# Kernel optimization log

Hardware: AMD Instinct MI355X
Metric: run time of the kernel (lower is better)

## Reference

```python
import jax, jax.numpy as jnp
import numpy as np

ALPHA = 0.2  # LeakyReLU negative slope
B, L, FIN, FOUT = 128, 512, 128, 128

def setup_inputs() -> dict:
    key = jax.random.key(0)
    k1, k2, k3, k4, k5 = jax.random.split(key, 5)
    h = jax.random.normal(k1, (B, L, FIN), jnp.float32)
    W = jax.random.normal(k2, (FIN, FOUT), jnp.float32) * (1.0 / np.sqrt(FIN))
    a = jax.random.normal(k3, (2 * FOUT,), jnp.float32) * (1.0 / np.sqrt(2 * FOUT))
    edge_bias = jax.random.normal(k4, (B, L, L), jnp.float32) * 0.1
    adj_mask = jax.random.uniform(k5, (L, L)) > 0.3
    adj_mask = adj_mask | jnp.eye(L, dtype=bool)  # self-loops avoid fully-masked rows
    return {"h": h, "W": W, "a": a, "edge_bias": edge_bias, "adj_mask": adj_mask}

def reference(h, W, a, edge_bias, adj_mask):
    # Wh: [B, L, Fout]
    Wh = jnp.einsum('blf,fo->blo', h, W)
    Fout = W.shape[1]
    # a([Wh_i, Wh_j]) == Wh_i @ a[:Fout] + Wh_j @ a[Fout:]  (avoids O(B*L*L*2F) concat)
    ei = Wh @ a[:Fout]   # [B, L]  (target i contribution)
    ej = Wh @ a[Fout:]   # [B, L]  (source j contribution)
    e = jax.nn.leaky_relu(ei[:, :, None] + ej[:, None, :], ALPHA) + edge_bias  # [B, L, L]
    e = jnp.where(adj_mask[None, :, :], e, -jnp.inf)
    att = jax.nn.softmax(e, axis=-1)  # dropout=0.0 -> identity
    h_prime = jnp.einsum('bij,bjo->bio', att, Wh)  # [B, L, Fout]
    return jax.nn.elu(h_prime)  # concat=True branch
```

## Files before the change

### kernel.cpp

```cpp
#include <hip/hip_runtime.h>
#include <string.h>

#define ALPHA 0.2f

typedef short short8 __attribute__((ext_vector_type(8)));
typedef float floatx4 __attribute__((ext_vector_type(4)));
typedef int intx4 __attribute__((ext_vector_type(4)));
typedef unsigned short ushort4v __attribute__((ext_vector_type(4)));

__device__ inline unsigned short f2bf(float f) {
    unsigned int v; __builtin_memcpy(&v, &f, 4);
    v = v + 0x7FFFu + ((v >> 16) & 1u);
    return (unsigned short)(v >> 16);
}

__device__ inline floatx4 ntload_f4(const float* p) {
    return __builtin_nontemporal_load((const floatx4*)p);
}

__global__ __launch_bounds__(256) void wh_kernel(const float* __restrict__ h,
                                                 const float* __restrict__ W,
                                                 const float* __restrict__ a,
                                                 unsigned short* __restrict__ wht,
                                                 float* __restrict__ ei,
                                                 float* __restrict__ ej)
{
    __shared__ __align__(16) unsigned short h_s[128][136];
    __shared__ __align__(16) unsigned short w_s[128][136];
    __shared__ float a_s[256];
    const int tid  = threadIdx.x;
    const int lane = tid & 63;
    const int wv   = tid >> 6;
    const int quad = lane >> 4;
    const int l16  = lane & 15;
    const int r0   = blockIdx.x * 128;
    const int b    = r0 >> 9;
    const int jb   = r0 & 511;

    const float* hbase = h + (size_t)r0 * 128;
    for (int it = 0; it < 16; ++it) {
        int idx4 = it * 256 + tid;
        floatx4 v = *(const floatx4*)(hbase + idx4 * 4);
        int row = idx4 >> 5;
        int col = (idx4 & 31) * 4;
        ushort4v u;
        for (int e = 0; e < 4; ++e) u[e] = f2bf(v[e]);
        *(ushort4v*)&h_s[row][col] = u;
    }
    for (int it = 0; it < 64; ++it) {
        int idx = it * 256 + tid;
        w_s[idx & 127][idx >> 7] = f2bf(W[idx]);
    }
    a_s[tid] = a[tid];
    __syncthreads();

    floatx4 acc[8][2];
    for (int mo = 0; mo < 8; ++mo)
        for (int n = 0; n < 2; ++n) acc[mo][n] = (floatx4)0.f;

    for (int kk = 0; kk < 4; ++kk) {
        short8 bfr[2];
        for (int n = 0; n < 2; ++n)
            bfr[n] = *(const short8*)&h_s[wv * 32 + n * 16 + l16][kk * 32 + quad * 8];
        for (int mo = 0; mo < 8; ++mo) {
            short8 afr = *(const short8*)&w_s[mo * 16 + l16][kk * 32 + quad * 8];
            acc[mo][0] = __builtin_amdgcn_mfma_f32_16x16x32_bf16(afr, bfr[0], acc[mo][0], 0, 0, 0);
            acc[mo][1] = __builtin_amdgcn_mfma_f32_16x16x32_bf16(afr, bfr[1], acc[mo][1], 0, 0, 0);
        }
    }

    for (int n = 0; n < 2; ++n) {
        float si = 0.f, sj = 0.f;
        for (int mo = 0; mo < 8; ++mo)
            for (int r = 0; r < 4; ++r) {
                int o = mo * 16 + quad * 4 + r;
                float v = acc[mo][n][r];
                si += v * a_s[o];
                sj += v * a_s[128 + o];
            }
        si += __shfl_xor(si, 16); si += __shfl_xor(si, 32);
        sj += __shfl_xor(sj, 16); sj += __shfl_xor(sj, 32);
        if (quad == 0) {
            int j = jb + wv * 32 + n * 16 + l16;
            ei[b * 512 + j] = si;
            ej[b * 512 + j] = sj;
        }
    }

    for (int mo = 0; mo < 8; ++mo)
        for (int n = 0; n < 2; ++n)
            for (int r = 0; r < 4; ++r) {
                int o = mo * 16 + quad * 4 + r;
                int j = jb + wv * 32 + n * 16 + l16;
                wht[(size_t)b * 65536 + o * 512 + j] = f2bf(acc[mo][n][r]);
            }
}

__global__ __launch_bounds__(512, 4) void attn_kernel(const unsigned short* __restrict__ wht,
                                                      const float* __restrict__ ei,
                                                      const float* __restrict__ ej,
                                                      const float* __restrict__ bias,
                                                      const int* __restrict__ adj,
                                                      float* __restrict__ out)
{
    __shared__ __align__(16) unsigned short p_s[64][520];
    __shared__ float ei_s[64];
    __shared__ float s_row[64];

    const int tid  = threadIdx.x;
    const int lane = tid & 63;
    const int wv   = tid >> 6;
    const int quad = lane >> 4;
    const int l16  = lane & 15;

    const int n  = blockIdx.x;
    const int x  = n & 7;
    const int r  = n >> 3;
    const int b  = x * 16 + (r >> 3);
    const int i0 = (r & 7) * 64;

    const float* bp = bias + ((size_t)(b * 512 + i0 + wv * 8)) * 512;
    const int*   ap = adj + (i0 + wv * 8) * 512;
    floatx4 bb0 = ntload_f4(bp + lane * 4);
    floatx4 bb1 = ntload_f4(bp + 256 + lane * 4);
    intx4   mm0 = *(const intx4*)(ap + lane * 4);
    intx4   mm1 = *(const intx4*)(ap + 256 + lane * 4);

    const floatx4 ejv0 = *(const floatx4*)(ej + b * 512 + lane * 4);
    const floatx4 ejv1 = *(const floatx4*)(ej + b * 512 + 256 + lane * 4);
    if (tid < 64) ei_s[tid] = ei[b * 512 + i0 + tid];
    __syncthreads();

    float rsum[8];

#pragma unroll
    for (int rr = 0; rr < 8; ++rr) {
        floatx4 nb0, nb1; intx4 nm0, nm1;
        if (rr < 7) {
            nb0 = ntload_f4(bp + 512 + lane * 4);
            nb1 = ntload_f4(bp + 768 + lane * 4);
            nm0 = *(const intx4*)(ap + 512 + lane * 4);
            nm1 = *(const intx4*)(ap + 768 + lane * 4);
        }
        const int il = wv * 8 + rr;
        const float eiv = ei_s[il];
        float sm = 0.f;
        ushort4v p0, p1;
#pragma unroll
        for (int e = 0; e < 4; ++e) {
            float xv = eiv + ejv0[e];
            xv = fmaxf(xv, ALPHA * xv);
            xv += bb0[e];
            float p = __expf(xv);
            p = (mm0[e] != 0) ? p : 0.f;
            sm += p;
            p0[e] = f2bf(p);
        }
#pragma unroll
        for (int e = 0; e < 4; ++e) {
            float xv = eiv + ejv1[e];
            xv = fmaxf(xv, ALPHA * xv);
            xv += bb1[e];
            float p = __expf(xv);
            p = (mm1[e] != 0) ? p : 0.f;
            sm += p;
            p1[e] = f2bf(p);
        }
        *(ushort4v*)&p_s[il][lane * 4]       = p0;
        *(ushort4v*)&p_s[il][256 + lane * 4] = p1;
        rsum[rr] = sm;
        bb0 = nb0; bb1 = nb1; mm0 = nm0; mm1 = nm1;
        bp += 512; ap += 512;
    }

#pragma unroll
    for (int rr = 0; rr < 8; ++rr)
        for (int off = 32; off; off >>= 1)
            rsum[rr] += __shfl_xor(rsum[rr], off);
    if (lane == 0)
#pragma unroll
        for (int rr = 0; rr < 8; ++rr) s_row[wv * 8 + rr] = rsum[rr];
    __syncthreads();

    floatx4 acc[4];
#pragma unroll
    for (int m = 0; m < 4; ++m) acc[m] = (floatx4)0.f;

    const unsigned short* wb = wht + (size_t)b * 65536 + (wv * 16 + l16) * 512 + quad * 8;
    short8 bf = *(const short8*)(wb);
#pragma unroll
    for (int k16 = 0; k16 < 16; ++k16) {
        int ko = k16 * 32 + quad * 8;
        short8 nbf;
        if (k16 < 15) nbf = *(const short8*)(wb + (k16 + 1) * 32);
        short8 af0 = *(const short8*)&p_s[l16][ko];
        short8 af1 = *(const short8*)&p_s[16 + l16][ko];
        short8 af2 = *(const short8*)&p_s[32 + l16][ko];
        short8 af3 = *(const short8*)&p_s[48 + l16][ko];
        acc[0] = __builtin_amdgcn_mfma_f32_16x16x32_bf16(af0, bf, acc[0], 0, 0, 0);
        acc[1] = __builtin_amdgcn_mfma_f32_16x16x32_bf16(af1, bf, acc[1], 0, 0, 0);
        acc[2] = __builtin_amdgcn_mfma_f32_16x16x32_bf16(af2, bf, acc[2], 0, 0, 0);
        acc[3] = __builtin_amdgcn_mfma_f32_16x16x32_bf16(af3, bf, acc[3], 0, 0, 0);
        bf = nbf;
    }

#pragma unroll
    for (int m = 0; m < 4; ++m)
#pragma unroll
        for (int rr2 = 0; rr2 < 4; ++rr2) {
            int il = m * 16 + quad * 4 + rr2;
            int o  = wv * 16 + l16;
            float v = acc[m][rr2] / s_row[il];
            v = v > 0.f ? v : (__expf(v) - 1.f);
            __builtin_nontemporal_store(v, &out[((size_t)(b * 512 + i0 + il)) * 128 + o]);
        }
}

extern "C" void kernel_launch(void* const* d_in, const int* in_sizes, int n_in,
                              void* d_out, int out_size, void* d_ws, size_t ws_size,
                              hipStream_t stream)
{
    const float* h    = (const float*)d_in[0];
    const float* W    = (const float*)d_in[1];
    const float* a    = (const float*)d_in[2];
    const float* bias = (const float*)d_in[3];
    const int*   adj  = (const int*)d_in[4];
    float*       out  = (float*)d_out;

    unsigned short* wht = (unsigned short*)d_ws;
    float* ei = (float*)((char*)d_ws + 16777216);
    float* ej = ei + 65536;

    hipLaunchKernelGGL(wh_kernel,   dim3(512),  dim3(256), 0, stream, h, W, a, wht, ei, ej);
    hipLaunchKernelGGL(attn_kernel, dim3(1024), dim3(512), 0, stream, wht, ei, ej, bias, adj, out);
}
```

Baseline: 248.9 us.

## Bit-pack adjacency mask, deepen bias prefetch, and load h directly in wh_kernel

The wh_kernel now also packs the int adjacency matrix into a per-row bitmask using ballots, so attn_kernel reads 64 bytes per row of mask from LDS instead of 2KB of ints per row from global memory. The bias loads in attn_kernel switch to inline-asm nontemporal dwordx4 loads with a 4-deep ring buffer and explicit vmcnt waits, which keeps more bytes in flight. ej is staged through shared memory. In wh_kernel, h is loaded straight into registers with a software prefetch instead of being staged in LDS. The risks are the manual waitcnt bookkeeping, which depends on compiler ordering, and the extra workspace region used for the mask.

```diff
diff --git a/kernel.cpp b/kernel.cpp
--- a/kernel.cpp
+++ b/kernel.cpp
@@ -5,7 +5,6 @@
 
 typedef short short8 __attribute__((ext_vector_type(8)));
 typedef float floatx4 __attribute__((ext_vector_type(4)));
-typedef int intx4 __attribute__((ext_vector_type(4)));
 typedef unsigned short ushort4v __attribute__((ext_vector_type(4)));
 
 __device__ inline unsigned short f2bf(float f) {
@@ -14,18 +13,17 @@
     return (unsigned short)(v >> 16);
 }
 
-__device__ inline floatx4 ntload_f4(const float* p) {
-    return __builtin_nontemporal_load((const floatx4*)p);
-}
-
-__global__ __launch_bounds__(256) void wh_kernel(const float* __restrict__ h,
-                                                 const float* __restrict__ W,
-                                                 const float* __restrict__ a,
-                                                 unsigned short* __restrict__ wht,
-                                                 float* __restrict__ ei,
-                                                 float* __restrict__ ej)
+#define GLD4(dst, p) asm volatile("global_load_dwordx4 %0, %1, off nt" : "=v"(dst) : "v"(p))
+
+__global__ __launch_bounds__(256, 4) void wh_kernel(const float* __restrict__ h,
+                                                    const float* __restrict__ W,
+                                                    const float* __restrict__ a,
+                                                    const int* __restrict__ adj,
+                                                    unsigned short* __restrict__ wht,
+                                                    float* __restrict__ ei,
+                                                    float* __restrict__ ej,
+                                                    unsigned long long* __restrict__ mask)
 {
-    __shared__ __align__(16) unsigned short h_s[128][136];
     __shared__ __align__(16) unsigned short w_s[128][136];
     __shared__ float a_s[256];
     const int tid  = threadIdx.x;
@@ -37,36 +35,61 @@
     const int b    = r0 >> 9;
     const int jb   = r0 & 511;
 
-    const float* hbase = h + (size_t)r0 * 128;
-    for (int it = 0; it < 16; ++it) {
-        int idx4 = it * 256 + tid;
-        floatx4 v = *(const floatx4*)(hbase + idx4 * 4);
-        int row = idx4 >> 5;
-        int col = (idx4 & 31) * 4;
-        ushort4v u;
-        for (int e = 0; e < 4; ++e) u[e] = f2bf(v[e]);
-        *(ushort4v*)&h_s[row][col] = u;
-    }
     for (int it = 0; it < 64; ++it) {
         int idx = it * 256 + tid;
         w_s[idx & 127][idx >> 7] = f2bf(W[idx]);
     }
     a_s[tid] = a[tid];
+
+    if (blockIdx.x < 128) {
+        const int row = blockIdx.x * 4 + wv;
+        const int* ar = adj + row * 512;
+        unsigned long long wbits[8];
+#pragma unroll
+        for (int q = 0; q < 8; ++q) wbits[q] = __ballot(ar[q * 64 + lane] != 0);
+        if (lane == 0) {
+            unsigned long long* mr = mask + row * 8;
+#pragma unroll
+            for (int q = 0; q < 8; ++q) mr[q] = wbits[q];
+        }
+    }
     __syncthreads();
+
+    const float* hp0 = h + (size_t)(r0 + wv * 32 + l16) * 128 + quad * 8;
+    const float* hp1 = hp0 + 16 * 128;
 
     floatx4 acc[8][2];
     for (int mo = 0; mo < 8; ++mo)
         for (int n = 0; n < 2; ++n) acc[mo][n] = (floatx4)0.f;
 
+    floatx4 c00 = *(const floatx4*)(hp0);
+    floatx4 c01 = *(const floatx4*)(hp0 + 4);
+    floatx4 c10 = *(const floatx4*)(hp1);
+    floatx4 c11 = *(const floatx4*)(hp1 + 4);
+#pragma unroll
     for (int kk = 0; kk < 4; ++kk) {
-        short8 bfr[2];
-        for (int n = 0; n < 2; ++n)
-            bfr[n] = *(const short8*)&h_s[wv * 32 + n * 16 + l16][kk * 32 + quad * 8];
+        floatx4 n00, n01, n10, n11;
+        if (kk < 3) {
+            n00 = *(const floatx4*)(hp0 + (kk + 1) * 32);
+            n01 = *(const floatx4*)(hp0 + (kk + 1) * 32 + 4);
+            n10 = *(const floatx4*)(hp1 + (kk + 1) * 32);
+            n11 = *(const floatx4*)(hp1 + (kk + 1) * 32 + 4);
+        }
+        short8 bfr0, bfr1;
+#pragma unroll
+        for (int e = 0; e < 4; ++e) {
+            bfr0[e]     = (short)f2bf(c00[e]);
+            bfr0[4 + e] = (short)f2bf(c01[e]);
+            bfr1[e]     = (short)f2bf(c10[e]);
+            bfr1[4 + e] = (short)f2bf(c11[e]);
+        }
+#pragma unroll
         for (int mo = 0; mo < 8; ++mo) {
             short8 afr = *(const short8*)&w_s[mo * 16 + l16][kk * 32 + quad * 8];
-            acc[mo][0] = __builtin_amdgcn_mfma_f32_16x16x32_bf16(afr, bfr[0], acc[mo][0], 0, 0, 0);
-            acc[mo][1] = __builtin_amdgcn_mfma_f32_16x16x32_bf16(afr, bfr[1], acc[mo][1], 0, 0, 0);
-        }
+            acc[mo][0] = __builtin_amdgcn_mfma_f32_16x16x32_bf16(afr, bfr0, acc[mo][0], 0, 0, 0);
+            acc[mo][1] = __builtin_amdgcn_mfma_f32_16x16x32_bf16(afr, bfr1, acc[mo][1], 0, 0, 0);
+        }
+        c00 = n00; c01 = n01; c10 = n10; c11 = n11;
     }
 
     for (int n = 0; n < 2; ++n) {
@@ -100,12 +123,14 @@
                                                       const float* __restrict__ ei,
                                                       const float* __restrict__ ej,
                                                       const float* __restrict__ bias,
-                                                      const int* __restrict__ adj,
+                                                      const unsigned* __restrict__ mask32,
                                                       float* __restrict__ out)
 {
     __shared__ __align__(16) unsigned short p_s[64][520];
     __shared__ float ei_s[64];
+    __shared__ float ej_s[512];
     __shared__ float s_row[64];
+    __shared__ unsigned m_s[64][16];
 
     const int tid  = threadIdx.x;
     const int lane = tid & 63;
@@ -119,40 +144,51 @@
     const int b  = x * 16 + (r >> 3);
     const int i0 = (r & 7) * 64;
 
+    ej_s[tid] = ej[b * 512 + tid];
+    if (tid < 64) ei_s[tid] = ei[b * 512 + i0 + tid];
+#pragma unroll
+    for (int it = 0; it < 2; ++it) {
+        int idx = it * 512 + tid;
+        m_s[idx >> 4][idx & 15] = mask32[i0 * 16 + idx];
+    }
+    __syncthreads();
+
     const float* bp = bias + ((size_t)(b * 512 + i0 + wv * 8)) * 512;
-    const int*   ap = adj + (i0 + wv * 8) * 512;
-    floatx4 bb0 = ntload_f4(bp + lane * 4);
-    floatx4 bb1 = ntload_f4(bp + 256 + lane * 4);
-    intx4   mm0 = *(const intx4*)(ap + lane * 4);
-    intx4   mm1 = *(const intx4*)(ap + 256 + lane * 4);
-
-    const floatx4 ejv0 = *(const floatx4*)(ej + b * 512 + lane * 4);
-    const floatx4 ejv1 = *(const floatx4*)(ej + b * 512 + 256 + lane * 4);
-    if (tid < 64) ei_s[tid] = ei[b * 512 + i0 + tid];
-    __syncthreads();
+    const int mw = lane >> 3;
+    const int ms = (lane & 7) * 4;
+
+    const floatx4 ejv0 = *(const floatx4*)&ej_s[lane * 4];
+    const floatx4 ejv1 = *(const floatx4*)&ej_s[256 + lane * 4];
+
+    floatx4 q0[4], q1[4];
+    GLD4(q0[0], bp + lane * 4);            GLD4(q1[0], bp + 256 + lane * 4);
+    GLD4(q0[1], bp + 512 + lane * 4);      GLD4(q1[1], bp + 768 + lane * 4);
+    GLD4(q0[2], bp + 1024 + lane * 4);     GLD4(q1[2], bp + 1280 + lane * 4);
+    GLD4(q0[3], bp + 1536 + lane * 4);     GLD4(q1[3], bp + 1792 + lane * 4);
 
     float rsum[8];
-
 #pragma unroll
     for (int rr = 0; rr < 8; ++rr) {
-        floatx4 nb0, nb1; intx4 nm0, nm1;
-        if (rr < 7) {
-            nb0 = ntload_f4(bp + 512 + lane * 4);
-            nb1 = ntload_f4(bp + 768 + lane * 4);
-            nm0 = *(const intx4*)(ap + 512 + lane * 4);
-            nm1 = *(const intx4*)(ap + 768 + lane * 4);
-        }
+        if (rr <= 4)      asm volatile("s_waitcnt vmcnt(6)" ::: "memory");
+        else if (rr == 5) asm volatile("s_waitcnt vmcnt(4)" ::: "memory");
+        else if (rr == 6) asm volatile("s_waitcnt vmcnt(2)" ::: "memory");
+        else              asm volatile("s_waitcnt vmcnt(0)" ::: "memory");
+        __builtin_amdgcn_sched_barrier(0);
+
+        const int s  = rr & 3;
         const int il = wv * 8 + rr;
         const float eiv = ei_s[il];
+        const unsigned nib0 = (m_s[il][mw]     >> ms) & 0xFu;
+        const unsigned nib1 = (m_s[il][8 + mw] >> ms) & 0xFu;
         float sm = 0.f;
         ushort4v p0, p1;
 #pragma unroll
         for (int e = 0; e < 4; ++e) {
             float xv = eiv + ejv0[e];
             xv = fmaxf(xv, ALPHA * xv);
-            xv += bb0[e];
+            xv += q0[s][e];
             float p = __expf(xv);
-            p = (mm0[e] != 0) ? p : 0.f;
+            p = (nib0 & (1u << e)) ? p : 0.f;
             sm += p;
             p0[e] = f2bf(p);
         }
@@ -160,17 +196,20 @@
         for (int e = 0; e < 4; ++e) {
             float xv = eiv + ejv1[e];
             xv = fmaxf(xv, ALPHA * xv);
-            xv += bb1[e];
+            xv += q1[s][e];
             float p = __expf(xv);
-            p = (mm1[e] != 0) ? p : 0.f;
+            p = (nib1 & (1u << e)) ? p : 0.f;
             sm += p;
             p1[e] = f2bf(p);
         }
         *(ushort4v*)&p_s[il][lane * 4]       = p0;
         *(ushort4v*)&p_s[il][256 + lane * 4] = p1;
         rsum[rr] = sm;
-        bb0 = nb0; bb1 = nb1; mm0 = nm0; mm1 = nm1;
-        bp += 512; ap += 512;
+
+        if (rr < 4) {
+            GLD4(q0[s], bp + (size_t)(rr + 4) * 512 + lane * 4);
+            GLD4(q1[s], bp + (size_t)(rr + 4) * 512 + 256 + lane * 4);
+        }
     }
 
 #pragma unroll
@@ -230,7 +269,9 @@
     unsigned short* wht = (unsigned short*)d_ws;
     float* ei = (float*)((char*)d_ws + 16777216);
     float* ej = ei + 65536;
-
-    hipLaunchKernelGGL(wh_kernel,   dim3(512),  dim3(256), 0, stream, h, W, a, wht, ei, ej);
-    hipLaunchKernelGGL(attn_kernel, dim3(1024), dim3(512), 0, stream, wht, ei, ej, bias, adj, out);
-}
+    unsigned long long* mask = (unsigned long long*)((char*)d_ws + 17301504);
+
+    hipLaunchKernelGGL(wh_kernel,   dim3(512),  dim3(256), 0, stream, h, W, a, adj, wht, ei, ej, mask);
+    hipLaunchKernelGGL(attn_kernel, dim3(1024), dim3(512), 0, stream, wht, ei, ej, bias,
+                       (const unsigned*)mask, out);
+}
```

Result: faster. 241.5 us (-3.0%).
